# Kernel tuning notes

Hardware: AMD Instinct MI355X
Metric: run time of the kernel (lower is better)

## Reference

```python
import jax, jax.numpy as jnp
import numpy as np

NUM_CLS = 81
N_ROI = 512
N_POS = 128
OUT = 7
SAMP = 2
SCALES = (0.25, 0.125, 0.0625, 0.03125)


def _roi_align(feat, rois, out, scale, samp=SAMP):
    # feat: [C,H,W]; rois: [N,4] (x1,y1,x2,y2) in image coords. torchvision-style
    # ROIAlign, aligned=False, avg pool over samp x samp bilinear samples per bin.
    C, H, W = feat.shape
    b = rois * scale
    x1, y1, x2, y2 = b[:, 0], b[:, 1], b[:, 2], b[:, 3]
    bw = jnp.maximum(x2 - x1, 1.0) / out
    bh = jnp.maximum(y2 - y1, 1.0) / out
    N = rois.shape[0]
    # sample offsets within a roi, in bin units: [out, samp]
    grid = jnp.arange(out, dtype=feat.dtype)[:, None] + (jnp.arange(samp, dtype=feat.dtype)[None, :] + 0.5) / samp
    px = x1[:, None, None] + grid[None] * bw[:, None, None]  # [N,out,samp]
    py = y1[:, None, None] + grid[None] * bh[:, None, None]
    # full sampling grid [N, out_y, out_x, samp_y, samp_x]
    PX = jnp.broadcast_to(px[:, None, :, None, :], (N, out, out, samp, samp))
    PY = jnp.broadcast_to(py[:, :, None, :, None], (N, out, out, samp, samp))
    valid = (PX > -1.0) & (PX < W) & (PY > -1.0) & (PY < H)
    x = jnp.clip(PX, 0.0, W - 1.0)
    y = jnp.clip(PY, 0.0, H - 1.0)
    x0f = jnp.floor(x)
    y0f = jnp.floor(y)
    lx = x - x0f
    ly = y - y0f
    x0 = x0f.astype(jnp.int32)
    y0 = y0f.astype(jnp.int32)
    x1i = jnp.minimum(x0 + 1, W - 1)
    y1i = jnp.minimum(y0 + 1, H - 1)
    def g(yi, xi):
        return feat[:, yi, xi]  # [C,N,out,out,samp,samp]
    v = (g(y0, x0) * (1 - ly) * (1 - lx) + g(y0, x1i) * (1 - ly) * lx
         + g(y1i, x0) * ly * (1 - lx) + g(y1i, x1i) * ly * lx)
    v = v * valid.astype(feat.dtype)
    pooled = v.mean(axis=(-1, -2))  # [C,N,out,out]
    return pooled.transpose(1, 0, 2, 3)  # [N,C,out,out]


def setup_inputs() -> dict:
    key = jax.random.key(0)
    ks = jax.random.split(key, 16)
    H_IMG, W_IMG = 800.0, 1024.0
    P2 = jax.random.normal(ks[0], (1, 256, 200, 256), jnp.float32)
    P3 = jax.random.normal(ks[1], (1, 256, 100, 128), jnp.float32)
    P4 = jax.random.normal(ks[2], (1, 256, 50, 64), jnp.float32)
    P5 = jax.random.normal(ks[3], (1, 256, 25, 32), jnp.float32)
    x1 = jax.random.uniform(ks[4], (N_ROI,)) * (W_IMG - 64.0)
    y1 = jax.random.uniform(ks[5], (N_ROI,)) * (H_IMG - 64.0)
    w = jax.random.uniform(ks[6], (N_ROI,), minval=16.0, maxval=512.0)
    h = jax.random.uniform(ks[7], (N_ROI,), minval=16.0, maxval=512.0)
    rois = jnp.stack([x1, y1, jnp.minimum(x1 + w, W_IMG - 1.0), jnp.minimum(y1 + h, H_IMG - 1.0)], axis=-1)
    label = jax.random.randint(ks[8], (N_ROI,), 0, NUM_CLS, dtype=jnp.int32)
    loc = jax.random.normal(ks[9], (N_POS, 4), jnp.float32) * 0.1
    s = 0.02
    return {
        'P2': P2, 'P3': P3, 'P4': P4, 'P5': P5,
        'rois': rois, 'label': label, 'loc': loc,
        'W1': jax.random.normal(ks[10], (256 * OUT * OUT, 1024), jnp.float32) * s,
        'b1': jnp.zeros((1024,), jnp.float32),
        'W2': jax.random.normal(ks[11], (1024, 1024), jnp.float32) * s,
        'b2': jnp.zeros((1024,), jnp.float32),
        'Wcls': jax.random.normal(ks[12], (1024, NUM_CLS), jnp.float32) * s,
        'bcls': jnp.zeros((NUM_CLS,), jnp.float32),
        'Wloc': jax.random.normal(ks[13], (1024, NUM_CLS * 4), jnp.float32) * s,
        'bloc': jnp.zeros((NUM_CLS * 4,), jnp.float32),
    }


def reference(P2, P3, P4, P5, rois, label, loc, W1, b1, W2, b2, Wcls, bcls, Wloc, bloc):
    feats = (P2[0], P3[0], P4[0], P5[0])
    # FPN level assignment: floor(4 + log2(sqrt(area)/224)).clamp(2,5) - 2
    area = (rois[:, 2] - rois[:, 0] + 1.0) * (rois[:, 3] - rois[:, 1] + 1.0)
    lvl = jnp.floor(4.0 + jnp.log(jnp.sqrt(area) / 224.0) / np.log(2.0))
    lvl = (jnp.clip(lvl, 2.0, 5.0) - 2.0).astype(jnp.int32)  # [N] in {0,1,2,3}
    onehot = jax.nn.one_hot(lvl, 4, dtype=rois.dtype)  # [N,4]
    # pool every roi at all 4 levels, select assigned level (same values as
    # the original per-level grouping + argsort re-ordering)
    pooled = jnp.stack([_roi_align(f, rois, OUT, s) for f, s in zip(feats, SCALES)])  # [4,N,C,7,7]
    x = jnp.einsum('lnchw,nl->nchw', pooled, onehot)
    # Fast head
    x = x.reshape(x.shape[0], -1)
    h = jax.nn.relu(x @ W1 + b1)
    h = jax.nn.relu(h @ W2 + b2)
    logits = h @ Wcls + bcls                    # [N, num_cls]
    locp = (h @ Wloc + bloc).reshape(-1, NUM_CLS, 4)
    # loss assembly
    logp = jax.nn.log_softmax(logits, axis=-1)
    cls_loss = -jnp.take_along_axis(logp, label[:, None], axis=1).mean()
    loc_train = locp[jnp.arange(N_POS), label[:N_POS]]  # class-indexed gather
    t = jnp.abs(loc_train - loc)
    sl1 = jnp.where(t < 1.0, 0.5 * t * t, t - 0.5)  # SmoothL1, sigma=1
    box_loss = sl1.sum() / float(N_ROI)
    return cls_loss + box_loss
```

## Files before the change

### kernel.cpp

```cpp
#include <hip/hip_runtime.h>
#include <hip/hip_bf16.h>
#include <math.h>

#define N_ROI 512
#define N_POS 128
#define NUM_CLS 81
#define KDIM 12544
#define HID 1024

typedef __bf16 bf16x8 __attribute__((ext_vector_type(8)));
typedef __bf16 bf16x4 __attribute__((ext_vector_type(4)));
typedef float f32x4 __attribute__((ext_vector_type(4)));

__device__ inline void gload16(const void* g, void* lds) {
  __builtin_amdgcn_global_load_lds(
      (const __attribute__((address_space(1))) void*)g,
      (__attribute__((address_space(3))) void*)lds, 16, 0, 0);
}

__global__ __launch_bounds__(256, 3) void roi_align_kernel(
    const float* __restrict__ P2, const float* __restrict__ P3,
    const float* __restrict__ P4, const float* __restrict__ P5,
    const float* __restrict__ rois, __bf16* __restrict__ xout) {
  int n = blockIdx.x;
  int t = threadIdx.x;

  __shared__ int    gxo[14];
  __shared__ float2 gxf[14];
  __shared__ int2   gyi[14];
  __shared__ float2 gyf[14];
  __shared__ int    s_lvl, s_HWb;

  float rx1 = rois[n * 4 + 0], ry1 = rois[n * 4 + 1];
  float rx2 = rois[n * 4 + 2], ry2 = rois[n * 4 + 3];
  float area = (rx2 - rx1 + 1.0f) * (ry2 - ry1 + 1.0f);
  float lf = floorf(4.0f + log2f(sqrtf(area) / 224.0f));
  lf = fminf(fmaxf(lf, 2.0f), 5.0f);
  int lvl = (int)lf - 2;

  const float scales[4] = {0.25f, 0.125f, 0.0625f, 0.03125f};
  const int   Hs[4] = {200, 100, 50, 25};
  const int   Ws[4] = {256, 128, 64, 32};
  float sc = scales[lvl];
  int H = Hs[lvl], W = Ws[lvl];

  float bx1 = rx1 * sc, by1 = ry1 * sc;
  float bw = fmaxf(rx2 * sc - bx1, 1.0f) * (1.0f / 7.0f);
  float bh = fmaxf(ry2 * sc - by1, 1.0f) * (1.0f / 7.0f);

  if (t < 14) {
    int i = t >> 1, j = t & 1;
    float g = (float)i + 0.25f + 0.5f * (float)j;
    float px = bx1 + g * bw;
    float vx = (px > -1.0f && px < (float)W) ? 1.0f : 0.0f;
    float xx = fminf(fmaxf(px, 0.0f), (float)(W - 1));
    float x0f = floorf(xx);
    int x0 = (int)x0f;
    int xa = min(x0, W - 2);
    gxo[t] = xa * 4;
    gxf[t] = make_float2((x0 > xa) ? 1.0f : (xx - x0f), vx);
    if (t == 0) { s_lvl = lvl; s_HWb = H * W * 4; }
  } else if (t >= 64 && t < 78) {
    int s = t - 64;
    int i = s >> 1, j = s & 1;
    float g = (float)i + 0.25f + 0.5f * (float)j;
    float py = by1 + g * bh;
    float vy = (py > -1.0f && py < (float)H) ? 1.0f : 0.0f;
    float yy = fminf(fmaxf(py, 0.0f), (float)(H - 1));
    float y0f = floorf(yy);
    int y0 = (int)y0f;
    int y1 = min(y0 + 1, H - 1);
    gyi[s] = make_int2(y0 * W * 4, y1 * W * 4);
    gyf[s] = make_float2(yy - y0f, vy);
  }
  __syncthreads();

  int lvl_s = __builtin_amdgcn_readfirstlane(s_lvl);
  const char* base = (const char*)(lvl_s == 0 ? P2 : lvl_s == 1 ? P3
                                   : lvl_s == 2 ? P4 : P5);
  int HWb = s_HWb;

  int wave = t >> 6, lane = t & 63;
  if (lane >= 49) return;

  int oh = (lane * 37) >> 8;
  int ow = lane - oh * 7;

  int2   xo = *(const int2*)&gxo[2 * ow];
  float4 xf = *(const float4*)&gxf[2 * ow];
  int4   yi = *(const int4*)&gyi[2 * oh];
  float4 yf = *(const float4*)&gyf[2 * oh];

  int off[8];
  off[0] = yi.x + xo.x; off[1] = yi.y + xo.x;
  off[2] = yi.x + xo.y; off[3] = yi.y + xo.y;
  off[4] = yi.z + xo.x; off[5] = yi.w + xo.x;
  off[6] = yi.z + xo.y; off[7] = yi.w + xo.y;

  float w00 = yf.y * xf.y, w01 = yf.y * xf.w;
  float w10 = yf.w * xf.y, w11 = yf.w * xf.w;

  int c0 = blockIdx.y * 32 + wave * 8;
  const char* bc0 = base + (size_t)c0 * HWb;

  float2 g[8][8];
#pragma unroll
  for (int ch = 0; ch < 8; ++ch) {
    const char* bcc = bc0 + (size_t)ch * HWb;
#pragma unroll
    for (int l = 0; l < 8; ++l)
      g[ch][l] = *(const float2*)(bcc + off[l]);
  }
  __builtin_amdgcn_sched_barrier(0);

  __bf16* outp = xout + (size_t)n * KDIM + (size_t)c0 * 49 + lane;
#pragma unroll
  for (int ch = 0; ch < 8; ++ch) {
    float fa, fb, s = 0.0f;
    fa = g[ch][0].x + xf.x * (g[ch][0].y - g[ch][0].x);
    fb = g[ch][1].x + xf.x * (g[ch][1].y - g[ch][1].x);
    s += (fa + yf.x * (fb - fa)) * w00;
    fa = g[ch][2].x + xf.z * (g[ch][2].y - g[ch][2].x);
    fb = g[ch][3].x + xf.z * (g[ch][3].y - g[ch][3].x);
    s += (fa + yf.x * (fb - fa)) * w01;
    fa = g[ch][4].x + xf.x * (g[ch][4].y - g[ch][4].x);
    fb = g[ch][5].x + xf.x * (g[ch][5].y - g[ch][5].x);
    s += (fa + yf.z * (fb - fa)) * w10;
    fa = g[ch][6].x + xf.z * (g[ch][6].y - g[ch][6].x);
    fb = g[ch][7].x + xf.z * (g[ch][7].y - g[ch][7].x);
    s += (fa + yf.z * (fb - fa)) * w11;
    outp[ch * 49] = (__bf16)(s * 0.25f);
  }
}

__global__ __launch_bounds__(256) void transpose_kernel(
    const float* __restrict__ W1, __bf16* __restrict__ W1t,
    const float* __restrict__ W2, __bf16* __restrict__ W2t,
    const float* __restrict__ Wcls, __bf16* __restrict__ WcT) {
  __shared__ float tile[64][65];
  int bid = blockIdx.x;
  int t = threadIdx.x;

  const float* src;
  __bf16* dst;
  int R, C, bcb, brb;
  bool pad_cls = false;
  if (bid < 3136) {
    src = W1; dst = W1t; R = KDIM; C = HID;
    bcb = (bid & 15) * 64; brb = (bid >> 4) * 64;
  } else if (bid < 3392) {
    int id = bid - 3136;
    src = W2; dst = W2t; R = HID; C = HID;
    bcb = (id & 15) * 64; brb = (id >> 4) * 64;
  } else {
    int id = bid - 3392;
    src = Wcls; dst = WcT; R = HID; C = 128;
    bcb = (id >> 4) * 64; brb = (id & 15) * 64;
    pad_cls = true;
  }

  int rr = t >> 4, c4 = (t & 15) * 4;
  if (!pad_cls) {
#pragma unroll
    for (int p = 0; p < 4; ++p) {
      int r = p * 16 + rr;
      f32x4 v = *(const f32x4*)&src[(size_t)(brb + r) * C + bcb + c4];
      tile[r][c4] = v.x; tile[r][c4 + 1] = v.y;
      tile[r][c4 + 2] = v.z; tile[r][c4 + 3] = v.w;
    }
  } else {
#pragma unroll
    for (int p = 0; p < 4; ++p) {
      int r = p * 16 + rr;
#pragma unroll
      for (int i = 0; i < 4; ++i) {
        int j = bcb + c4 + i;
        tile[r][c4 + i] =
            (j < NUM_CLS) ? src[(size_t)(brb + r) * NUM_CLS + j] : 0.0f;
      }
    }
  }
  __syncthreads();
#pragma unroll
  for (int p = 0; p < 2; ++p) {
    int group = t + 256 * p;
    int c = group >> 3;
    int r0 = (group & 7) * 8;
    bf16x8 o;
#pragma unroll
    for (int j = 0; j < 8; ++j) o[j] = (__bf16)tile[r0 + j][c];
    *(bf16x8*)&dst[(size_t)(bcb + c) * R + brb + r0] = o;
  }
}

__global__ __launch_bounds__(256, 2) void mfma_gemm128(
    const __bf16* __restrict__ A, const __bf16* __restrict__ Bt,
    float* __restrict__ part, int M, int N, int K, int chunk) {
  __shared__ __align__(16) unsigned char smem[16384];
  unsigned char* As = smem;
  unsigned char* Bs = smem + 8192;

  int t = threadIdx.x;
  int wave = t >> 6;
  int lane = t & 63;
  int fr = lane & 15, q = lane >> 4;
  int bm = blockIdx.y * 128, bn = blockIdx.x * 128;
  int wm = (wave >> 1) * 64, wn = (wave & 1) * 64;

  int kbeg = blockIdx.z * chunk;
  int kend = min(K, kbeg + chunk);

  int qsrc = ((t & 3) - ((t >> 3) & 3)) & 3;
  const __bf16* a0 = A + (size_t)(bm + (t >> 2)) * K + kbeg + qsrc * 8;
  const __bf16* a1 = a0 + (size_t)64 * K;
  const __bf16* b0 = Bt + (size_t)(bn + (t >> 2)) * K + kbeg + qsrc * 8;
  const __bf16* b1 = b0 + (size_t)64 * K;
  unsigned char* AsW = As + wave * 1024;
  unsigned char* BsW = Bs + wave * 1024;

  int sA = ((q + (fr >> 1)) & 3) * 16;

  f32x4 acc[4][4];
#pragma unroll
  for (int i = 0; i < 4; ++i)
#pragma unroll
    for (int j = 0; j < 4; ++j) acc[i][j] = (f32x4){0.f, 0.f, 0.f, 0.f};

  for (int k0 = kbeg; k0 < kend; k0 += 32) {
    __syncthreads();
    gload16(a0, AsW);
    gload16(a1, AsW + 4096);
    gload16(b0, BsW);
    gload16(b1, BsW + 4096);
    a0 += 32; a1 += 32; b0 += 32; b1 += 32;
    __syncthreads();

    bf16x8 af[4], bfr[4];
#pragma unroll
    for (int i = 0; i < 4; ++i)
      af[i] = *(const bf16x8*)(As + (wm + 16 * i + fr) * 64 + sA);
#pragma unroll
    for (int j = 0; j < 4; ++j)
      bfr[j] = *(const bf16x8*)(Bs + (wn + 16 * j + fr) * 64 + sA);
#pragma unroll
    for (int i = 0; i < 4; ++i)
#pragma unroll
      for (int j = 0; j < 4; ++j)
        acc[i][j] = __builtin_amdgcn_mfma_f32_16x16x32_bf16(af[i], bfr[j],
                                                            acc[i][j], 0, 0, 0);
  }

  float* P = part + (size_t)blockIdx.z * M * N;
#pragma unroll
  for (int i = 0; i < 4; ++i) {
#pragma unroll
    for (int j = 0; j < 4; ++j) {
      int row0 = bm + wm + 16 * i + q * 4;
      int col = bn + wn + 16 * j + fr;
#pragma unroll
      for (int r = 0; r < 4; ++r)
        P[(size_t)(row0 + r) * N + col] = acc[i][j][r];
    }
  }
}

__global__ __launch_bounds__(256) void reduce_kernel(
    const float* __restrict__ part, int S, int MN, int Nmask,
    const float* __restrict__ bias, int bias_n, int relu,
    float* __restrict__ outf, __bf16* __restrict__ outb) {
  int i4 = (blockIdx.x * 256 + threadIdx.x) * 4;
  if (i4 >= MN) return;
  f32x4 s = {0.f, 0.f, 0.f, 0.f};
  for (int z = 0; z < S; ++z) {
    f32x4 v = *(const f32x4*)&part[(size_t)z * MN + i4];
    s.x += v.x; s.y += v.y; s.z += v.z; s.w += v.w;
  }
  int col = i4 & Nmask;
  float r[4] = {s.x, s.y, s.z, s.w};
#pragma unroll
  for (int j = 0; j < 4; ++j) {
    float b = (col + j < bias_n) ? bias[col + j] : 0.0f;
    float v = r[j] + b;
    if (relu) v = fmaxf(v, 0.0f);
    r[j] = v;
  }
  if (outf) {
    f32x4 o = {r[0], r[1], r[2], r[3]};
    *(f32x4*)&outf[i4] = o;
  }
  if (outb) {
    bf16x4 o = {(__bf16)r[0], (__bf16)r[1], (__bf16)r[2], (__bf16)r[3]};
    *(bf16x4*)&outb[i4] = o;
  }
}

__global__ __launch_bounds__(256) void loc_head_kernel(
    const float* __restrict__ h2, const float* __restrict__ Wloc,
    const float* __restrict__ bloc, const int* __restrict__ label,
    float* __restrict__ loct) {
  int n = blockIdx.x;
  int d = threadIdx.x >> 6;
  int lane = threadIdx.x & 63;
  int lab = label[n];
  const float* h = h2 + (size_t)n * HID;
  const float* w = Wloc + (size_t)lab * 4 + d;
  float s = 0.0f;
#pragma unroll
  for (int i = 0; i < 16; ++i) {
    int k = lane + i * 64;
    s += h[k] * w[(size_t)k * (NUM_CLS * 4)];
  }
#pragma unroll
  for (int off = 32; off > 0; off >>= 1) s += __shfl_down(s, off);
  if (lane == 0) loct[n * 4 + d] = s + bloc[lab * 4 + d];
}

__global__ __launch_bounds__(512) void loss_kernel(
    const float* __restrict__ logits, const int* __restrict__ label,
    const float* __restrict__ loct, const float* __restrict__ loc,
    float* __restrict__ out) {
  int t = threadIdx.x;
  const float* row = logits + (size_t)t * 128;
  float m = -1e30f;
  for (int j = 0; j < NUM_CLS; ++j) m = fmaxf(m, row[j]);
  float se = 0.0f;
  for (int j = 0; j < NUM_CLS; ++j) se += expf(row[j] - m);
  float cl = (m + logf(se)) - row[label[t]];

  float a = fabsf(loct[t] - loc[t]);
  float bl = (a < 1.0f) ? 0.5f * a * a : a - 0.5f;

  float v = cl + bl;
#pragma unroll
  for (int off = 32; off > 0; off >>= 1) v += __shfl_down(v, off);

  __shared__ float red[8];
  if ((t & 63) == 0) red[t >> 6] = v;
  __syncthreads();
  if (t == 0) {
    float tot = 0.0f;
    for (int i = 0; i < 8; ++i) tot += red[i];
    out[0] = tot * (1.0f / (float)N_ROI);
  }
}

extern "C" void kernel_launch(void* const* d_in, const int* in_sizes, int n_in,
                              void* d_out, int out_size, void* d_ws, size_t ws_size,
                              hipStream_t stream) {
  const float* P2   = (const float*)d_in[0];
  const float* P3   = (const float*)d_in[1];
  const float* P4   = (const float*)d_in[2];
  const float* P5   = (const float*)d_in[3];
  const float* rois = (const float*)d_in[4];
  const int*   label= (const int*)d_in[5];
  const float* loc  = (const float*)d_in[6];
  const float* W1   = (const float*)d_in[7];
  const float* b1   = (const float*)d_in[8];
  const float* W2   = (const float*)d_in[9];
  const float* b2   = (const float*)d_in[10];
  const float* Wcls = (const float*)d_in[11];
  const float* bcls = (const float*)d_in[12];
  const float* Wloc = (const float*)d_in[13];
  const float* bloc = (const float*)d_in[14];
  float* out = (float*)d_out;

  char* w = (char*)d_ws;
  __bf16* xb  = (__bf16*)w;  w += (size_t)N_ROI * KDIM * 2;
  __bf16* W1t = (__bf16*)w;  w += (size_t)KDIM * HID * 2;
  __bf16* W2t = (__bf16*)w;  w += (size_t)HID * HID * 2;
  __bf16* WcT = (__bf16*)w;  w += (size_t)128 * HID * 2;
  __bf16* h1b = (__bf16*)w;  w += (size_t)N_ROI * HID * 2;
  __bf16* h2b = (__bf16*)w;  w += (size_t)N_ROI * HID * 2;
  float*  h2f = (float*)w;   w += (size_t)N_ROI * HID * 4;
  float*  logits = (float*)w; w += (size_t)N_ROI * 128 * 4;
  float*  loct = (float*)w;  w += (size_t)N_ROI * 4;
  float*  part = (float*)w;

  roi_align_kernel<<<dim3(N_ROI, 8), 256, 0, stream>>>(P2, P3, P4, P5, rois,
                                                       xb);
  transpose_kernel<<<3424, 256, 0, stream>>>(W1, W1t, W2, W2t, Wcls, WcT);

  mfma_gemm128<<<dim3(HID / 128, N_ROI / 128, 16), 256, 0, stream>>>(
      xb, W1t, part, N_ROI, HID, KDIM, 800);
  reduce_kernel<<<(N_ROI * HID) / 1024, 256, 0, stream>>>(
      part, 16, N_ROI * HID, HID - 1, b1, HID, 1, nullptr, h1b);

  mfma_gemm128<<<dim3(HID / 128, N_ROI / 128, 8), 256, 0, stream>>>(
      h1b, W2t, part, N_ROI, HID, HID, 128);
  reduce_kernel<<<(N_ROI * HID) / 1024, 256, 0, stream>>>(
      part, 8, N_ROI * HID, HID - 1, b2, HID, 1, h2f, h2b);

  mfma_gemm128<<<dim3(1, N_ROI / 128, 8), 256, 0, stream>>>(
      h2b, WcT, part, N_ROI, 128, HID, 128);
  reduce_kernel<<<(N_ROI * 128) / 1024, 256, 0, stream>>>(
      part, 8, N_ROI * 128, 127, bcls, NUM_CLS, 0, logits, nullptr);

  loc_head_kernel<<<N_POS, 256, 0, stream>>>(h2f, Wloc, bloc, label, loct);
  loss_kernel<<<1, 512, 0, stream>>>(logits, label, loct, loc, out);
}
```

Measured before the change: 288.9 us.

## Fuse all stages into one persistent kernel with grid-wide atomic barriers

Replaces the ten separate launches (roi align, transpose, three GEMMs with split-K reduces, loc head, loss) with one persistent kernel of 512 blocks. The stages are separated by software grid barriers built on atomic counters, which are zeroed by a memset before launch. The goal is to remove per-launch overhead and the gaps between kernels, and to let ROI-align and the weight transpose share one work loop. The cost is that many blocks must stay co-resident for the barrier, and every block spins at each barrier. Register pressure also rises because a single kernel carries both the GEMM and the gather paths, and the class GEMM split-K changes from 8 to 16.

Measured after the change: 690.1 us. +138.8%, slower.

```diff
diff --git a/kernel.cpp b/kernel.cpp
--- a/kernel.cpp
+++ b/kernel.cpp
@@ -7,10 +7,21 @@
 #define NUM_CLS 81
 #define KDIM 12544
 #define HID 1024
+#define NBLK 512
 
 typedef __bf16 bf16x8 __attribute__((ext_vector_type(8)));
-typedef __bf16 bf16x4 __attribute__((ext_vector_type(4)));
 typedef float f32x4 __attribute__((ext_vector_type(4)));
+
+struct Params {
+  const float *P2, *P3, *P4, *P5, *rois;
+  const int* label;
+  const float* loc;
+  const float *W1, *b1, *W2, *b2, *Wcls, *bcls, *Wloc, *bloc;
+  __bf16 *xb, *W1t, *W2t, *WcT, *h1b, *h2b;
+  float *h2f, *logits, *loct, *out;
+  unsigned* bar;
+  float* part;
+};
 
 __device__ inline void gload16(const void* g, void* lds) {
   __builtin_amdgcn_global_load_lds(
@@ -18,21 +29,31 @@
       (__attribute__((address_space(3))) void*)lds, 16, 0, 0);
 }
 
-__global__ __launch_bounds__(256, 3) void roi_align_kernel(
-    const float* __restrict__ P2, const float* __restrict__ P3,
-    const float* __restrict__ P4, const float* __restrict__ P5,
-    const float* __restrict__ rois, __bf16* __restrict__ xout) {
-  int n = blockIdx.x;
+union __align__(16) SmU {
+  float tile[64][65];
+  unsigned char gemm[16384];
+};
+
+__device__ inline void gbar(unsigned* cnt) {
+  __syncthreads();
+  if (threadIdx.x == 0) {
+    __threadfence();
+    atomicAdd(cnt, 1u);
+    while (atomicAdd(cnt, 0u) < NBLK) __builtin_amdgcn_s_sleep(2);
+    __threadfence();
+  }
+  __syncthreads();
+}
+
+__device__ void roi_unit(int unit, const Params& p,
+                         int* gxo, float2* gxf, int2* gyi, float2* gyf,
+                         int* s_lvl, int* s_HWb) {
+  int n = unit & 511;
+  int grp = unit >> 9;
   int t = threadIdx.x;
 
-  __shared__ int    gxo[14];
-  __shared__ float2 gxf[14];
-  __shared__ int2   gyi[14];
-  __shared__ float2 gyf[14];
-  __shared__ int    s_lvl, s_HWb;
-
-  float rx1 = rois[n * 4 + 0], ry1 = rois[n * 4 + 1];
-  float rx2 = rois[n * 4 + 2], ry2 = rois[n * 4 + 3];
+  float rx1 = p.rois[n * 4 + 0], ry1 = p.rois[n * 4 + 1];
+  float rx2 = p.rois[n * 4 + 2], ry2 = p.rois[n * 4 + 3];
   float area = (rx2 - rx1 + 1.0f) * (ry2 - ry1 + 1.0f);
   float lf = floorf(4.0f + log2f(sqrtf(area) / 224.0f));
   lf = fminf(fmaxf(lf, 2.0f), 5.0f);
@@ -59,7 +80,7 @@
     int xa = min(x0, W - 2);
     gxo[t] = xa * 4;
     gxf[t] = make_float2((x0 > xa) ? 1.0f : (xx - x0f), vx);
-    if (t == 0) { s_lvl = lvl; s_HWb = H * W * 4; }
+    if (t == 0) { *s_lvl = lvl; *s_HWb = H * W * 4; }
   } else if (t >= 64 && t < 78) {
     int s = t - 64;
     int i = s >> 1, j = s & 1;
@@ -75,86 +96,79 @@
   }
   __syncthreads();
 
-  int lvl_s = __builtin_amdgcn_readfirstlane(s_lvl);
-  const char* base = (const char*)(lvl_s == 0 ? P2 : lvl_s == 1 ? P3
-                                   : lvl_s == 2 ? P4 : P5);
-  int HWb = s_HWb;
+  int lvl_s = __builtin_amdgcn_readfirstlane(*s_lvl);
+  const char* base = (const char*)(lvl_s == 0 ? p.P2 : lvl_s == 1 ? p.P3
+                                   : lvl_s == 2 ? p.P4 : p.P5);
+  int HWb = *s_HWb;
 
   int wave = t >> 6, lane = t & 63;
-  if (lane >= 49) return;
-
-  int oh = (lane * 37) >> 8;
-  int ow = lane - oh * 7;
-
-  int2   xo = *(const int2*)&gxo[2 * ow];
-  float4 xf = *(const float4*)&gxf[2 * ow];
-  int4   yi = *(const int4*)&gyi[2 * oh];
-  float4 yf = *(const float4*)&gyf[2 * oh];
-
-  int off[8];
-  off[0] = yi.x + xo.x; off[1] = yi.y + xo.x;
-  off[2] = yi.x + xo.y; off[3] = yi.y + xo.y;
-  off[4] = yi.z + xo.x; off[5] = yi.w + xo.x;
-  off[6] = yi.z + xo.y; off[7] = yi.w + xo.y;
-
-  float w00 = yf.y * xf.y, w01 = yf.y * xf.w;
-  float w10 = yf.w * xf.y, w11 = yf.w * xf.w;
-
-  int c0 = blockIdx.y * 32 + wave * 8;
-  const char* bc0 = base + (size_t)c0 * HWb;
-
-  float2 g[8][8];
-#pragma unroll
-  for (int ch = 0; ch < 8; ++ch) {
-    const char* bcc = bc0 + (size_t)ch * HWb;
-#pragma unroll
-    for (int l = 0; l < 8; ++l)
-      g[ch][l] = *(const float2*)(bcc + off[l]);
-  }
-  __builtin_amdgcn_sched_barrier(0);
-
-  __bf16* outp = xout + (size_t)n * KDIM + (size_t)c0 * 49 + lane;
-#pragma unroll
-  for (int ch = 0; ch < 8; ++ch) {
-    float fa, fb, s = 0.0f;
-    fa = g[ch][0].x + xf.x * (g[ch][0].y - g[ch][0].x);
-    fb = g[ch][1].x + xf.x * (g[ch][1].y - g[ch][1].x);
-    s += (fa + yf.x * (fb - fa)) * w00;
-    fa = g[ch][2].x + xf.z * (g[ch][2].y - g[ch][2].x);
-    fb = g[ch][3].x + xf.z * (g[ch][3].y - g[ch][3].x);
-    s += (fa + yf.x * (fb - fa)) * w01;
-    fa = g[ch][4].x + xf.x * (g[ch][4].y - g[ch][4].x);
-    fb = g[ch][5].x + xf.x * (g[ch][5].y - g[ch][5].x);
-    s += (fa + yf.z * (fb - fa)) * w10;
-    fa = g[ch][6].x + xf.z * (g[ch][6].y - g[ch][6].x);
-    fb = g[ch][7].x + xf.z * (g[ch][7].y - g[ch][7].x);
-    s += (fa + yf.z * (fb - fa)) * w11;
-    outp[ch * 49] = (__bf16)(s * 0.25f);
-  }
-}
-
-__global__ __launch_bounds__(256) void transpose_kernel(
-    const float* __restrict__ W1, __bf16* __restrict__ W1t,
-    const float* __restrict__ W2, __bf16* __restrict__ W2t,
-    const float* __restrict__ Wcls, __bf16* __restrict__ WcT) {
-  __shared__ float tile[64][65];
-  int bid = blockIdx.x;
+  if (lane < 49) {
+    int oh = (lane * 37) >> 8;
+    int ow = lane - oh * 7;
+
+    int2   xo = *(const int2*)&gxo[2 * ow];
+    float4 xf = *(const float4*)&gxf[2 * ow];
+    int4   yi = *(const int4*)&gyi[2 * oh];
+    float4 yf = *(const float4*)&gyf[2 * oh];
+
+    int off[8];
+    off[0] = yi.x + xo.x; off[1] = yi.y + xo.x;
+    off[2] = yi.x + xo.y; off[3] = yi.y + xo.y;
+    off[4] = yi.z + xo.x; off[5] = yi.w + xo.x;
+    off[6] = yi.z + xo.y; off[7] = yi.w + xo.y;
+
+    float w00 = yf.y * xf.y, w01 = yf.y * xf.w;
+    float w10 = yf.w * xf.y, w11 = yf.w * xf.w;
+
+    int c0 = grp * 32 + wave * 8;
+    const char* bc0 = base + (size_t)c0 * HWb;
+
+    float2 g[8][8];
+#pragma unroll
+    for (int ch = 0; ch < 8; ++ch) {
+      const char* bcc = bc0 + (size_t)ch * HWb;
+#pragma unroll
+      for (int l = 0; l < 8; ++l)
+        g[ch][l] = *(const float2*)(bcc + off[l]);
+    }
+
+    __bf16* outp = p.xb + (size_t)n * KDIM + (size_t)c0 * 49 + lane;
+#pragma unroll
+    for (int ch = 0; ch < 8; ++ch) {
+      float fa, fb, s = 0.0f;
+      fa = g[ch][0].x + xf.x * (g[ch][0].y - g[ch][0].x);
+      fb = g[ch][1].x + xf.x * (g[ch][1].y - g[ch][1].x);
+      s += (fa + yf.x * (fb - fa)) * w00;
+      fa = g[ch][2].x + xf.z * (g[ch][2].y - g[ch][2].x);
+      fb = g[ch][3].x + xf.z * (g[ch][3].y - g[ch][3].x);
+      s += (fa + yf.x * (fb - fa)) * w01;
+      fa = g[ch][4].x + xf.x * (g[ch][4].y - g[ch][4].x);
+      fb = g[ch][5].x + xf.x * (g[ch][5].y - g[ch][5].x);
+      s += (fa + yf.z * (fb - fa)) * w10;
+      fa = g[ch][6].x + xf.z * (g[ch][6].y - g[ch][6].x);
+      fb = g[ch][7].x + xf.z * (g[ch][7].y - g[ch][7].x);
+      s += (fa + yf.z * (fb - fa)) * w11;
+      outp[ch * 49] = (__bf16)(s * 0.25f);
+    }
+  }
+}
+
+__device__ void transpose_unit(int bid, const Params& p, SmU& sm) {
   int t = threadIdx.x;
-
   const float* src;
   __bf16* dst;
   int R, C, bcb, brb;
   bool pad_cls = false;
   if (bid < 3136) {
-    src = W1; dst = W1t; R = KDIM; C = HID;
+    src = p.W1; dst = p.W1t; R = KDIM; C = HID;
     bcb = (bid & 15) * 64; brb = (bid >> 4) * 64;
   } else if (bid < 3392) {
     int id = bid - 3136;
-    src = W2; dst = W2t; R = HID; C = HID;
+    src = p.W2; dst = p.W2t; R = HID; C = HID;
     bcb = (id & 15) * 64; brb = (id >> 4) * 64;
   } else {
     int id = bid - 3392;
-    src = Wcls; dst = WcT; R = HID; C = 128;
+    src = p.Wcls; dst = p.WcT; R = HID; C = 128;
     bcb = (id >> 4) * 64; brb = (id & 15) * 64;
     pad_cls = true;
   }
@@ -162,52 +176,51 @@
   int rr = t >> 4, c4 = (t & 15) * 4;
   if (!pad_cls) {
 #pragma unroll
-    for (int p = 0; p < 4; ++p) {
-      int r = p * 16 + rr;
+    for (int q = 0; q < 4; ++q) {
+      int r = q * 16 + rr;
       f32x4 v = *(const f32x4*)&src[(size_t)(brb + r) * C + bcb + c4];
-      tile[r][c4] = v.x; tile[r][c4 + 1] = v.y;
-      tile[r][c4 + 2] = v.z; tile[r][c4 + 3] = v.w;
+      sm.tile[r][c4] = v.x; sm.tile[r][c4 + 1] = v.y;
+      sm.tile[r][c4 + 2] = v.z; sm.tile[r][c4 + 3] = v.w;
     }
   } else {
 #pragma unroll
-    for (int p = 0; p < 4; ++p) {
-      int r = p * 16 + rr;
+    for (int q = 0; q < 4; ++q) {
+      int r = q * 16 + rr;
 #pragma unroll
       for (int i = 0; i < 4; ++i) {
         int j = bcb + c4 + i;
-        tile[r][c4 + i] =
+        sm.tile[r][c4 + i] =
             (j < NUM_CLS) ? src[(size_t)(brb + r) * NUM_CLS + j] : 0.0f;
       }
     }
   }
   __syncthreads();
 #pragma unroll
-  for (int p = 0; p < 2; ++p) {
-    int group = t + 256 * p;
+  for (int q = 0; q < 2; ++q) {
+    int group = t + 256 * q;
     int c = group >> 3;
     int r0 = (group & 7) * 8;
     bf16x8 o;
 #pragma unroll
-    for (int j = 0; j < 8; ++j) o[j] = (__bf16)tile[r0 + j][c];
+    for (int j = 0; j < 8; ++j) o[j] = (__bf16)sm.tile[r0 + j][c];
     *(bf16x8*)&dst[(size_t)(bcb + c) * R + brb + r0] = o;
   }
 }
 
-__global__ __launch_bounds__(256, 2) void mfma_gemm128(
-    const __bf16* __restrict__ A, const __bf16* __restrict__ Bt,
-    float* __restrict__ part, int M, int N, int K, int chunk) {
-  __shared__ __align__(16) unsigned char smem[16384];
-  unsigned char* As = smem;
-  unsigned char* Bs = smem + 8192;
+__device__ void gemm_tile(const __bf16* A, const __bf16* Bt, float* part,
+                          int M, int N, int K, int tm, int tn, int z,
+                          int chunk, SmU& sm) {
+  unsigned char* As = sm.gemm;
+  unsigned char* Bs = sm.gemm + 8192;
 
   int t = threadIdx.x;
   int wave = t >> 6;
   int lane = t & 63;
   int fr = lane & 15, q = lane >> 4;
-  int bm = blockIdx.y * 128, bn = blockIdx.x * 128;
+  int bm = tm * 128, bn = tn * 128;
   int wm = (wave >> 1) * 64, wn = (wave & 1) * 64;
 
-  int kbeg = blockIdx.z * chunk;
+  int kbeg = z * chunk;
   int kend = min(K, kbeg + chunk);
 
   int qsrc = ((t & 3) - ((t >> 3) & 3)) & 3;
@@ -250,7 +263,7 @@
                                                             acc[i][j], 0, 0, 0);
   }
 
-  float* P = part + (size_t)blockIdx.z * M * N;
+  float* P = part + (size_t)z * M * N;
 #pragma unroll
   for (int i = 0; i < 4; ++i) {
 #pragma unroll
@@ -264,11 +277,10 @@
   }
 }
 
-__global__ __launch_bounds__(256) void reduce_kernel(
-    const float* __restrict__ part, int S, int MN, int Nmask,
-    const float* __restrict__ bias, int bias_n, int relu,
-    float* __restrict__ outf, __bf16* __restrict__ outb) {
-  int i4 = (blockIdx.x * 256 + threadIdx.x) * 4;
+__device__ void reduce_unit(int qidx, const float* part, int S, int MN,
+                            int Nmask, const float* bias, int bias_n, int relu,
+                            float* outf, __bf16* outb) {
+  int i4 = qidx * 4;
   if (i4 >= MN) return;
   f32x4 s = {0.f, 0.f, 0.f, 0.f};
   for (int z = 0; z < S; ++z) {
@@ -289,21 +301,17 @@
     *(f32x4*)&outf[i4] = o;
   }
   if (outb) {
-    bf16x4 o = {(__bf16)r[0], (__bf16)r[1], (__bf16)r[2], (__bf16)r[3]};
-    *(bf16x4*)&outb[i4] = o;
-  }
-}
-
-__global__ __launch_bounds__(256) void loc_head_kernel(
-    const float* __restrict__ h2, const float* __restrict__ Wloc,
-    const float* __restrict__ bloc, const int* __restrict__ label,
-    float* __restrict__ loct) {
-  int n = blockIdx.x;
+    __bf16 o[4] = {(__bf16)r[0], (__bf16)r[1], (__bf16)r[2], (__bf16)r[3]};
+    *(double*)&outb[i4] = *(double*)o;
+  }
+}
+
+__device__ void loc_unit(int n, const Params& p) {
   int d = threadIdx.x >> 6;
   int lane = threadIdx.x & 63;
-  int lab = label[n];
-  const float* h = h2 + (size_t)n * HID;
-  const float* w = Wloc + (size_t)lab * 4 + d;
+  int lab = p.label[n];
+  const float* h = p.h2f + (size_t)n * HID;
+  const float* w = p.Wloc + (size_t)lab * 4 + d;
   float s = 0.0f;
 #pragma unroll
   for (int i = 0; i < 16; ++i) {
@@ -312,89 +320,125 @@
   }
 #pragma unroll
   for (int off = 32; off > 0; off >>= 1) s += __shfl_down(s, off);
-  if (lane == 0) loct[n * 4 + d] = s + bloc[lab * 4 + d];
-}
-
-__global__ __launch_bounds__(512) void loss_kernel(
-    const float* __restrict__ logits, const int* __restrict__ label,
-    const float* __restrict__ loct, const float* __restrict__ loc,
-    float* __restrict__ out) {
+  if (lane == 0) p.loct[n * 4 + d] = s + p.bloc[lab * 4 + d];
+}
+
+__device__ void loss_unit(const Params& p) {
+  __shared__ float red[4];
   int t = threadIdx.x;
-  const float* row = logits + (size_t)t * 128;
-  float m = -1e30f;
-  for (int j = 0; j < NUM_CLS; ++j) m = fmaxf(m, row[j]);
-  float se = 0.0f;
-  for (int j = 0; j < NUM_CLS; ++j) se += expf(row[j] - m);
-  float cl = (m + logf(se)) - row[label[t]];
-
-  float a = fabsf(loct[t] - loc[t]);
-  float bl = (a < 1.0f) ? 0.5f * a * a : a - 0.5f;
-
-  float v = cl + bl;
+  float v = 0.0f;
+#pragma unroll
+  for (int rr = 0; rr < 2; ++rr) {
+    int r = t + rr * 256;
+    const float* row = p.logits + (size_t)r * 128;
+    float m = -1e30f;
+    for (int j = 0; j < NUM_CLS; ++j) m = fmaxf(m, row[j]);
+    float se = 0.0f;
+    for (int j = 0; j < NUM_CLS; ++j) se += expf(row[j] - m);
+    v += (m + logf(se)) - row[p.label[r]];
+    float a = fabsf(p.loct[r] - p.loc[r]);
+    v += (a < 1.0f) ? 0.5f * a * a : a - 0.5f;
+  }
 #pragma unroll
   for (int off = 32; off > 0; off >>= 1) v += __shfl_down(v, off);
-
-  __shared__ float red[8];
   if ((t & 63) == 0) red[t >> 6] = v;
   __syncthreads();
-  if (t == 0) {
-    float tot = 0.0f;
-    for (int i = 0; i < 8; ++i) tot += red[i];
-    out[0] = tot * (1.0f / (float)N_ROI);
-  }
+  if (t == 0)
+    p.out[0] = (red[0] + red[1] + red[2] + red[3]) * (1.0f / (float)N_ROI);
+}
+
+__global__ __launch_bounds__(256, 2) void mega_kernel(Params p) {
+  int b = blockIdx.x;
+  int t = threadIdx.x;
+
+  __shared__ SmU sm;
+  __shared__ int    gxo[14];
+  __shared__ float2 gxf[14];
+  __shared__ int2   gyi[14];
+  __shared__ float2 gyf[14];
+  __shared__ int    s_lvl, s_HWb;
+
+  for (int u = b; u < 7520; u += NBLK) {
+    if (u < 4096)
+      roi_unit(u, p, gxo, gxf, gyi, gyf, &s_lvl, &s_HWb);
+    else
+      transpose_unit(u - 4096, p, sm);
+    __syncthreads();
+  }
+  gbar(p.bar + 0);
+
+  for (int u = b; u < 512; u += NBLK)
+    gemm_tile(p.xb, p.W1t, p.part, N_ROI, HID, KDIM, u >> 7, (u >> 4) & 7,
+              u & 15, 800, sm);
+  gbar(p.bar + 16);
+
+  for (int q = b * 256 + t; q < (N_ROI * HID) / 4; q += NBLK * 256)
+    reduce_unit(q, p.part, 16, N_ROI * HID, HID - 1, p.b1, HID, 1, nullptr,
+                p.h1b);
+  gbar(p.bar + 32);
+
+  for (int u = b; u < 256; u += NBLK)
+    gemm_tile(p.h1b, p.W2t, p.part, N_ROI, HID, HID, u >> 6, (u >> 3) & 7,
+              u & 7, 128, sm);
+  gbar(p.bar + 48);
+
+  for (int q = b * 256 + t; q < (N_ROI * HID) / 4; q += NBLK * 256)
+    reduce_unit(q, p.part, 8, N_ROI * HID, HID - 1, p.b2, HID, 1, p.h2f,
+                p.h2b);
+  gbar(p.bar + 64);
+
+  for (int u = b; u < 64 + N_POS; u += NBLK) {
+    if (u < 64)
+      gemm_tile(p.h2b, p.WcT, p.part, N_ROI, 128, HID, u >> 4, 0, u & 15, 64,
+                sm);
+    else
+      loc_unit(u - 64, p);
+    __syncthreads();
+  }
+  gbar(p.bar + 80);
+
+  for (int q = b * 256 + t; q < (N_ROI * 128) / 4; q += NBLK * 256)
+    reduce_unit(q, p.part, 16, N_ROI * 128, 127, p.bcls, NUM_CLS, 0, p.logits,
+                nullptr);
+  gbar(p.bar + 96);
+
+  if (b == 0) loss_unit(p);
 }
 
 extern "C" void kernel_launch(void* const* d_in, const int* in_sizes, int n_in,
                               void* d_out, int out_size, void* d_ws, size_t ws_size,
                               hipStream_t stream) {
-  const float* P2   = (const float*)d_in[0];
-  const float* P3   = (const float*)d_in[1];
-  const float* P4   = (const float*)d_in[2];
-  const float* P5   = (const float*)d_in[3];
-  const float* rois = (const float*)d_in[4];
-  const int*   label= (const int*)d_in[5];
-  const float* loc  = (const float*)d_in[6];
-  const float* W1   = (const float*)d_in[7];
-  const float* b1   = (const float*)d_in[8];
-  const float* W2   = (const float*)d_in[9];
-  const float* b2   = (const float*)d_in[10];
-  const float* Wcls = (const float*)d_in[11];
-  const float* bcls = (const float*)d_in[12];
-  const float* Wloc = (const float*)d_in[13];
-  const float* bloc = (const float*)d_in[14];
-  float* out = (float*)d_out;
+  Params p;
+  p.P2   = (const float*)d_in[0];
+  p.P3   = (const float*)d_in[1];
+  p.P4   = (const float*)d_in[2];
+  p.P5   = (const float*)d_in[3];
+  p.rois = (const float*)d_in[4];
+  p.label= (const int*)d_in[5];
+  p.loc  = (const float*)d_in[6];
+  p.W1   = (const float*)d_in[7];
+  p.b1   = (const float*)d_in[8];
+  p.W2   = (const float*)d_in[9];
+  p.b2   = (const float*)d_in[10];
+  p.Wcls = (const float*)d_in[11];
+  p.bcls = (const float*)d_in[12];
+  p.Wloc = (const float*)d_in[13];
+  p.bloc = (const float*)d_in[14];
+  p.out  = (float*)d_out;
 
   char* w = (char*)d_ws;
-  __bf16* xb  = (__bf16*)w;  w += (size_t)N_ROI * KDIM * 2;
-  __bf16* W1t = (__bf16*)w;  w += (size_t)KDIM * HID * 2;
-  __bf16* W2t = (__bf16*)w;  w += (size_t)HID * HID * 2;
-  __bf16* WcT = (__bf16*)w;  w += (size_t)128 * HID * 2;
-  __bf16* h1b = (__bf16*)w;  w += (size_t)N_ROI * HID * 2;
-  __bf16* h2b = (__bf16*)w;  w += (size_t)N_ROI * HID * 2;
-  float*  h2f = (float*)w;   w += (size_t)N_ROI * HID * 4;
-  float*  logits = (float*)w; w += (size_t)N_ROI * 128 * 4;
-  float*  loct = (float*)w;  w += (size_t)N_ROI * 4;
-  float*  part = (float*)w;
-
-  roi_align_kernel<<<dim3(N_ROI, 8), 256, 0, stream>>>(P2, P3, P4, P5, rois,
-                                                       xb);
-  transpose_kernel<<<3424, 256, 0, stream>>>(W1, W1t, W2, W2t, Wcls, WcT);
-
-  mfma_gemm128<<<dim3(HID / 128, N_ROI / 128, 16), 256, 0, stream>>>(
-      xb, W1t, part, N_ROI, HID, KDIM, 800);
-  reduce_kernel<<<(N_ROI * HID) / 1024, 256, 0, stream>>>(
-      part, 16, N_ROI * HID, HID - 1, b1, HID, 1, nullptr, h1b);
-
-  mfma_gemm128<<<dim3(HID / 128, N_ROI / 128, 8), 256, 0, stream>>>(
-      h1b, W2t, part, N_ROI, HID, HID, 128);
-  reduce_kernel<<<(N_ROI * HID) / 1024, 256, 0, stream>>>(
-      part, 8, N_ROI * HID, HID - 1, b2, HID, 1, h2f, h2b);
-
-  mfma_gemm128<<<dim3(1, N_ROI / 128, 8), 256, 0, stream>>>(
-      h2b, WcT, part, N_ROI, 128, HID, 128);
-  reduce_kernel<<<(N_ROI * 128) / 1024, 256, 0, stream>>>(
-      part, 8, N_ROI * 128, 127, bcls, NUM_CLS, 0, logits, nullptr);
-
-  loc_head_kernel<<<N_POS, 256, 0, stream>>>(h2f, Wloc, bloc, label, loct);
-  loss_kernel<<<1, 512, 0, stream>>>(logits, label, loct, loc, out);
-}
+  p.xb  = (__bf16*)w;  w += (size_t)N_ROI * KDIM * 2;
+  p.W1t = (__bf16*)w;  w += (size_t)KDIM * HID * 2;
+  p.W2t = (__bf16*)w;  w += (size_t)HID * HID * 2;
+  p.WcT = (__bf16*)w;  w += (size_t)128 * HID * 2;
+  p.h1b = (__bf16*)w;  w += (size_t)N_ROI * HID * 2;
+  p.h2b = (__bf16*)w;  w += (size_t)N_ROI * HID * 2;
+  p.h2f = (float*)w;   w += (size_t)N_ROI * HID * 4;
+  p.logits = (float*)w; w += (size_t)N_ROI * 128 * 4;
+  p.loct = (float*)w;  w += (size_t)N_ROI * 4;
+  p.bar  = (unsigned*)w; w += 512;
+  p.part = (float*)w;
+
+  hipMemsetAsync(p.bar, 0, 512, stream);
+  mega_kernel<<<NBLK, 256, 0, stream>>>(p);
+}
```
